# Performance work log

Measured on AMD Instinct MI355X. Metric: run time of the kernel, lower is better.

## Reference

```python
import jax, jax.numpy as jnp
import numpy as np

N, T, D, H = 32, 1024, 512, 512


def setup_inputs() -> dict:
    key = jax.random.key(0)
    k1, k2, k3, k4 = jax.random.split(key, 4)
    x = jax.random.normal(k1, (N, T, D), dtype=jnp.float32)
    h0 = jax.random.normal(k2, (N, H), dtype=jnp.float32)
    Wx = jax.random.normal(k3, (D, 4 * H), dtype=jnp.float32) / np.sqrt(D)
    Wh = jax.random.normal(k4, (H, 4 * H), dtype=jnp.float32) / np.sqrt(H)
    b = jnp.zeros((4 * H,), dtype=jnp.float32)
    return {"x": x, "h0": h0, "Wx": Wx, "Wh": Wh, "b": b}


def reference(x, h0, Wx, Wh, b):
    Hdim = h0.shape[1]
    # Precompute input projection for all timesteps: (N,T,4H)
    xW = jnp.einsum('ntd,dk->ntk', x, Wx) + b

    def step(carry, xw_t):
        h, c = carry
        a = xw_t + h @ Wh  # (N,4H)
        i = jax.nn.sigmoid(a[:, :Hdim])
        f = jax.nn.sigmoid(a[:, Hdim:2 * Hdim])
        o = jax.nn.sigmoid(a[:, 2 * Hdim:3 * Hdim])
        g = jnp.tanh(a[:, 3 * Hdim:])
        c_next = f * c + i * g
        h_next = o * jnp.tanh(c_next)
        return (h_next, c_next), h_next

    c0 = jnp.zeros_like(h0)
    xW_t = jnp.swapaxes(xW, 0, 1)  # (T,N,4H) for scan over time
    _, hs = jax.lax.scan(step, (h0, c0), xW_t)
    return jnp.swapaxes(hs, 0, 1)  # (N,T,H)
```

## Files before the change

### kernel.cpp

```cpp
#include <hip/hip_runtime.h>
#include <hip/hip_bf16.h>


#define NWG 32
#define LDW 520
#define SMEM_BYTES (2*64*LDW*2 + 4*32*16*4 + 512*4)

typedef __attribute__((ext_vector_type(8))) short s16x8;
typedef __attribute__((ext_vector_type(4))) float f32x4;
typedef __attribute__((ext_vector_type(4))) float f4v;

__device__ __forceinline__ float b2f(unsigned short u) {
  unsigned v = ((unsigned)u) << 16;
  return __builtin_bit_cast(float, v);
}
__device__ __forceinline__ unsigned short f2b(float f) {
  unsigned u = __builtin_bit_cast(unsigned, f);
  unsigned r = (u + 0x7fffu + ((u >> 16) & 1u)) >> 16;
  return (unsigned short)r;
}
__device__ __forceinline__ float sigmoidf_(float x) {
  return 1.f / (1.f + __expf(-x));
}
__device__ __forceinline__ float tanhf_(float x) {
  float ax = fabsf(x);
  float e = __expf(-2.f * ax);
  float th = (1.f - e) / (1.f + e);
  return copysignf(th, x);
}

__device__ __forceinline__ void split8(const float* p, s16x8& hi, s16x8& lo) {
  float tmp[8];
  *(f4v*)&tmp[0] = *(const f4v*)&p[0];
  *(f4v*)&tmp[4] = *(const f4v*)&p[4];
#pragma unroll
  for (int j = 0; j < 8; j++) {
    unsigned short h = f2b(tmp[j]);
    hi[j] = (short)h;
    lo[j] = (short)f2b(tmp[j] - b2f(h));
  }
}
__device__ __forceinline__ s16x8 cvt8(const float* p) {
  float tmp[8];
  *(f4v*)&tmp[0] = *(const f4v*)&p[0];
  *(f4v*)&tmp[4] = *(const f4v*)&p[4];
  s16x8 r;
#pragma unroll
  for (int j = 0; j < 8; j++) r[j] = (short)f2b(tmp[j]);
  return r;
}

__device__ __forceinline__ bool sniff_is_bf16(const unsigned short* wx) {
  int cnt = 0;
  for (int i = 0; i < 512; i++) {
    unsigned e = (wx[i] >> 7) & 0xFF;
    cnt += (e >= 0x60 && e <= 0x9F) ? 1 : 0;
  }
  return cnt >= 440;
}

template <bool F32>
__device__ __forceinline__ void lstm_body(
    const void* xv, const void* h0v, const void* Wxv, const void* Whv,
    const void* biasv, void* outv, unsigned* __restrict__ bar,
    unsigned char* smem) {
  unsigned short* WhS = (unsigned short*)smem;
  unsigned short* WxS = (unsigned short*)(smem + 64 * LDW * 2);
  float* gatebuf = (float*)(smem + 2 * 64 * LDW * 2);
  float* cbuf = (float*)(smem + 2 * 64 * LDW * 2 + 4 * 32 * 16 * 4);

  const unsigned short* xb = (const unsigned short*)xv;
  const float* xf = (const float*)xv;
  const unsigned short* h0b = (const unsigned short*)h0v;
  const float* h0f = (const float*)h0v;

  const int tid = threadIdx.x;
  const int g = tid >> 6;
  const int lane = tid & 63;
  const int lm = lane & 15;
  const int q = lane >> 4;
  const int w = blockIdx.x;

  for (int i = 0; i < 8; i++) {
    int id = tid + i * 256;
    int gate = id & 3;
    int k = id >> 2;
    size_t base = (size_t)k * 2048 + gate * 512 + w * 16;
    if (F32) {
      const float* px = (const float*)Wxv + base;
      const float* ph = (const float*)Whv + base;
#pragma unroll
      for (int seg = 0; seg < 4; seg++) {
        f4v vx = *(const f4v*)(px + seg * 4);
        f4v vh = *(const f4v*)(ph + seg * 4);
#pragma unroll
        for (int j = 0; j < 4; j++) {
          WxS[(gate * 16 + seg * 4 + j) * LDW + k] = f2b(vx[j]);
          WhS[(gate * 16 + seg * 4 + j) * LDW + k] = f2b(vh[j]);
        }
      }
    } else {
      const unsigned short* px = (const unsigned short*)Wxv + base;
      const unsigned short* ph = (const unsigned short*)Whv + base;
      s16x8 vx0 = *(const s16x8*)&px[0];
      s16x8 vx1 = *(const s16x8*)&px[8];
      s16x8 vh0 = *(const s16x8*)&ph[0];
      s16x8 vh1 = *(const s16x8*)&ph[8];
#pragma unroll
      for (int j = 0; j < 8; j++) {
        WxS[(gate * 16 + j) * LDW + k]     = (unsigned short)vx0[j];
        WxS[(gate * 16 + 8 + j) * LDW + k] = (unsigned short)vx1[j];
        WhS[(gate * 16 + j) * LDW + k]     = (unsigned short)vh0[j];
        WhS[(gate * 16 + 8 + j) * LDW + k] = (unsigned short)vh1[j];
      }
    }
  }
  cbuf[tid] = 0.f;
  cbuf[tid + 256] = 0.f;

  float bv[2][4];
  for (int pp = 0; pp < 2; pp++) {
    int p = tid + pp * 256;
    int j = p & 15;
    for (int qq = 0; qq < 4; qq++) {
      int idx = qq * 512 + w * 16 + j;
      bv[pp][qq] = F32 ? ((const float*)biasv)[idx]
                       : b2f(((const unsigned short*)biasv)[idx]);
    }
  }
  __syncthreads();

  for (int t = 0; t < 1024; t++) {
    f32x4 acc0 = {0.f, 0.f, 0.f, 0.f};
    f32x4 acc1 = {0.f, 0.f, 0.f, 0.f};

    if (F32) {
      for (int kc = 0; kc < 16; kc++) {
        int k = kc * 32 + q * 8;
        s16x8 bfrag = *(const s16x8*)&WxS[(g * 16 + lm) * LDW + k];
        s16x8 a0 = cvt8(&xf[(size_t)(lm * 1024 + t) * 512 + k]);
        s16x8 a1 = cvt8(&xf[(size_t)((16 + lm) * 1024 + t) * 512 + k]);
        acc0 = __builtin_amdgcn_mfma_f32_16x16x32_bf16(a0, bfrag, acc0, 0, 0, 0);
        acc1 = __builtin_amdgcn_mfma_f32_16x16x32_bf16(a1, bfrag, acc1, 0, 0, 0);
      }
    } else {
      for (int kc = 0; kc < 16; kc++) {
        int k = kc * 32 + q * 8;
        s16x8 bfrag = *(const s16x8*)&WxS[(g * 16 + lm) * LDW + k];
        s16x8 a0 = *(const s16x8*)&xb[(size_t)(lm * 1024 + t) * 512 + k];
        s16x8 a1 = *(const s16x8*)&xb[(size_t)((16 + lm) * 1024 + t) * 512 + k];
        acc0 = __builtin_amdgcn_mfma_f32_16x16x32_bf16(a0, bfrag, acc0, 0, 0, 0);
        acc1 = __builtin_amdgcn_mfma_f32_16x16x32_bf16(a1, bfrag, acc1, 0, 0, 0);
      }
    }

    if (t > 0) {
      if (tid == 0) {
        const unsigned target = (unsigned)t * NWG;
        int guard = 0;
        while (__hip_atomic_load(bar, __ATOMIC_ACQUIRE,
                                 __HIP_MEMORY_SCOPE_AGENT) < target) {
          __builtin_amdgcn_s_sleep(1);
          if (++guard > (1 << 25)) break;
        }
      }
      __syncthreads();
    }

    if (F32) {
      float* outf = (float*)outv;
      const float* hpf = (t == 0) ? h0f : outf + (size_t)(t - 1) * 512;
      const size_t hstride = (t == 0) ? 512 : (size_t)1024 * 512;
      for (int kc = 0; kc < 16; kc++) {
        int k = kc * 32 + q * 8;
        s16x8 bfrag = *(const s16x8*)&WhS[(g * 16 + lm) * LDW + k];
        s16x8 hi0, lo0, hi1, lo1;
        split8(&hpf[lm * hstride + k], hi0, lo0);
        split8(&hpf[(16 + lm) * hstride + k], hi1, lo1);
        acc0 = __builtin_amdgcn_mfma_f32_16x16x32_bf16(hi0, bfrag, acc0, 0, 0, 0);
        acc0 = __builtin_amdgcn_mfma_f32_16x16x32_bf16(lo0, bfrag, acc0, 0, 0, 0);
        acc1 = __builtin_amdgcn_mfma_f32_16x16x32_bf16(hi1, bfrag, acc1, 0, 0, 0);
        acc1 = __builtin_amdgcn_mfma_f32_16x16x32_bf16(lo1, bfrag, acc1, 0, 0, 0);
      }
    } else {
      unsigned short* outb = (unsigned short*)outv;
      const unsigned short* hpb = (t == 0) ? h0b : outb + (size_t)(t - 1) * 512;
      const size_t hstride = (t == 0) ? 512 : (size_t)1024 * 512;
      for (int kc = 0; kc < 16; kc++) {
        int k = kc * 32 + q * 8;
        s16x8 bfrag = *(const s16x8*)&WhS[(g * 16 + lm) * LDW + k];
        s16x8 a0 = *(const s16x8*)&hpb[lm * hstride + k];
        s16x8 a1 = *(const s16x8*)&hpb[(16 + lm) * hstride + k];
        acc0 = __builtin_amdgcn_mfma_f32_16x16x32_bf16(a0, bfrag, acc0, 0, 0, 0);
        acc1 = __builtin_amdgcn_mfma_f32_16x16x32_bf16(a1, bfrag, acc1, 0, 0, 0);
      }
    }

    for (int r = 0; r < 4; r++) {
      gatebuf[(g * 32 + q * 4 + r) * 16 + lm] = acc0[r];
      gatebuf[(g * 32 + 16 + q * 4 + r) * 16 + lm] = acc1[r];
    }
    __syncthreads();

    for (int pp = 0; pp < 2; pp++) {
      int p = tid + pp * 256;
      int n = p >> 4, j = p & 15;
      float ai = gatebuf[(0 * 32 + n) * 16 + j] + bv[pp][0];
      float af = gatebuf[(1 * 32 + n) * 16 + j] + bv[pp][1];
      float ao = gatebuf[(2 * 32 + n) * 16 + j] + bv[pp][2];
      float ag = gatebuf[(3 * 32 + n) * 16 + j] + bv[pp][3];
      float iG = sigmoidf_(ai);
      float fG = sigmoidf_(af);
      float oG = sigmoidf_(ao);
      float gG = tanhf_(ag);
      float c = fG * cbuf[p] + iG * gG;
      cbuf[p] = c;
      float h = oG * tanhf_(c);
      size_t oidx = (size_t)(n * 1024 + t) * 512 + w * 16 + j;
      if (F32) ((float*)outv)[oidx] = h;
      else     ((unsigned short*)outv)[oidx] = f2b(h);
    }
    __syncthreads();

    if (t < 1023 && tid == 0) {
      __hip_atomic_fetch_add(bar, 1u, __ATOMIC_RELEASE,
                             __HIP_MEMORY_SCOPE_AGENT);
    }
  }
}

__global__ __launch_bounds__(256) void lstm_kernel(
    const void* x, const void* h0, const void* Wx, const void* Wh,
    const void* bias, void* out, unsigned* bar) {
  extern __shared__ unsigned char smem[];
  if (sniff_is_bf16((const unsigned short*)Wx))
    lstm_body<false>(x, h0, Wx, Wh, bias, out, bar, smem);
  else
    lstm_body<true>(x, h0, Wx, Wh, bias, out, bar, smem);
}

extern "C" void kernel_launch(void* const* d_in, const int* in_sizes, int n_in,
                              void* d_out, int out_size, void* d_ws, size_t ws_size,
                              hipStream_t stream) {
  const void* x  = d_in[0];
  const void* h0 = d_in[1];
  const void* Wx = d_in[2];
  const void* Wh = d_in[3];
  const void* b  = d_in[4];
  void* out = d_out;
  unsigned* bar = (unsigned*)d_ws;

  hipMemsetAsync(bar, 0, 128, stream);

  hipFuncSetAttribute((const void*)lstm_kernel,
                      hipFuncAttributeMaxDynamicSharedMemorySize, SMEM_BYTES);

  void* args[] = {(void*)&x, (void*)&h0, (void*)&Wx, (void*)&Wh,
                  (void*)&b, (void*)&out, (void*)&bar};
  hipLaunchCooperativeKernel((const void*)lstm_kernel, dim3(NWG), dim3(256),
                             args, SMEM_BYTES, stream);
}
```

Measured before the change: 21.63 ms.

## Replace atomic counter barrier with per-workgroup flags and system-coherent stores

Swaps the single atomic counter grid barrier for per-workgroup step flags. One wavefront polls all 32 flags with coherent loads and no sleep, and the hidden-state outputs and flags are written with sc0 sc1 stores so they bypass non-coherent caches. A buffer_inv is issued after the barrier so later reads see fresh data. The aim is lower barrier latency per timestep on this serial recurrence. In exchange it depends on inline asm memory ordering, and the poll guard is shorter, so a slow workgroup could let others run ahead on stale state.

```diff
diff --git a/kernel.cpp b/kernel.cpp
--- a/kernel.cpp
+++ b/kernel.cpp
@@ -27,6 +27,23 @@
   float e = __expf(-2.f * ax);
   float th = (1.f - e) / (1.f + e);
   return copysignf(th, x);
+}
+
+__device__ __forceinline__ void store_short_mall(void* p, unsigned short v) {
+  unsigned vv = v;
+  asm volatile("global_store_short %0, %1, off sc0 sc1"
+               :: "v"(p), "v"(vv) : "memory");
+}
+__device__ __forceinline__ void store_dword_mall(void* p, unsigned v) {
+  asm volatile("global_store_dword %0, %1, off sc0 sc1"
+               :: "v"(p), "v"(v) : "memory");
+}
+__device__ __forceinline__ unsigned load_dword_mall(const void* p) {
+  unsigned r;
+  asm volatile("global_load_dword %0, %1, off sc0 sc1\n\t"
+               "s_waitcnt vmcnt(0)"
+               : "=v"(r) : "v"(p) : "memory");
+  return r;
 }
 
 __device__ __forceinline__ void split8(const float* p, s16x8& hi, s16x8& lo) {
@@ -155,16 +172,18 @@
     }
 
     if (t > 0) {
-      if (tid == 0) {
-        const unsigned target = (unsigned)t * NWG;
+      if (tid < 64) {
+        const unsigned target = (unsigned)t;
+        const unsigned* fp = bar + (tid & 31);
         int guard = 0;
-        while (__hip_atomic_load(bar, __ATOMIC_ACQUIRE,
-                                 __HIP_MEMORY_SCOPE_AGENT) < target) {
-          __builtin_amdgcn_s_sleep(1);
-          if (++guard > (1 << 25)) break;
+        for (;;) {
+          unsigned v = load_dword_mall(fp);
+          if (__all(v >= target)) break;
+          if (++guard > (1 << 22)) break;
         }
       }
       __syncthreads();
+      asm volatile("buffer_inv sc1" ::: "memory");
     }
 
     if (F32) {
@@ -217,14 +236,16 @@
       cbuf[p] = c;
       float h = oG * tanhf_(c);
       size_t oidx = (size_t)(n * 1024 + t) * 512 + w * 16 + j;
-      if (F32) ((float*)outv)[oidx] = h;
-      else     ((unsigned short*)outv)[oidx] = f2b(h);
-    }
+      if (F32) store_dword_mall((float*)outv + oidx,
+                                __builtin_bit_cast(unsigned, h));
+      else     store_short_mall((unsigned short*)outv + oidx, f2b(h));
+    }
+    asm volatile("s_waitcnt vmcnt(0)" ::: "memory");
     __syncthreads();
 
     if (t < 1023 && tid == 0) {
-      __hip_atomic_fetch_add(bar, 1u, __ATOMIC_RELEASE,
-                             __HIP_MEMORY_SCOPE_AGENT);
+      unsigned done = (unsigned)(t + 1);
+      store_dword_mall(bar + w, done);
     }
   }
 }
```

New measurement: 23.02 ms. +6.4%, slower.
